# Kernel optimization log

Measured on AMD Instinct MI355X. Metric: run time of the kernel, lower is better.

The kernel has to match this reference:

```python
import jax, jax.numpy as jnp
import numpy as np
import math

NUM_HEADS = 16
CONSTITUENCY_PENALTY = 0.5
CONSTITUENT_BLOCK = 64  # deterministic stand-in for the ChomskyParser constituency spans


def constituency_penalty_mask(seq_len, dtype):
    # Tokens in the same constituent (contiguous block) attend freely;
    # cross-constituent pairs are penalized by CONSTITUENCY_PENALTY.
    blk = jnp.arange(seq_len) // CONSTITUENT_BLOCK
    return jnp.where(blk[:, None] != blk[None, :], CONSTITUENCY_PENALTY, 0.0).astype(dtype)


def setup_inputs() -> dict:
    key = jax.random.key(0)
    ks = jax.random.split(key, 7)
    B, S, H = 8, 1024, 1024
    scale = 1.0 / math.sqrt(H)
    return {
        "hidden_states": jax.random.normal(ks[0], (B, S, H), jnp.float32),
        "Wq": jax.random.normal(ks[1], (H, H), jnp.float32) * scale,
        "bq": jnp.zeros((H,), jnp.float32),
        "Wk": jax.random.normal(ks[2], (H, H), jnp.float32) * scale,
        "bk": jnp.zeros((H,), jnp.float32),
        "Wv": jax.random.normal(ks[3], (H, H), jnp.float32) * scale,
        "bv": jnp.zeros((H,), jnp.float32),
    }


def reference(hidden_states, Wq, bq, Wk, bk, Wv, bv):
    B, S, H = hidden_states.shape
    nh = NUM_HEADS
    hd = H // nh

    def heads(x):  # [B,S,H] -> [B,nh,S,hd]
        return x.reshape(B, S, nh, hd).transpose(0, 2, 1, 3)

    q = heads(hidden_states @ Wq + bq)
    k = heads(hidden_states @ Wk + bk)
    v = heads(hidden_states @ Wv + bv)

    scores = jnp.einsum("bhqd,bhkd->bhqk", q, k) / jnp.sqrt(jnp.asarray(hd, q.dtype))
    # constituency penalty subtracted before softmax (broadcast over batch, heads)
    scores = scores - constituency_penalty_mask(S, scores.dtype)[None, None, :, :]
    probs = jax.nn.softmax(scores, axis=-1)  # dropout is identity in eval

    ctx = jnp.einsum("bhqk,bhkd->bhqd", probs, v)
    ctx = ctx.transpose(0, 2, 1, 3).reshape(B, S, H)
    return ctx
```

## Files before the change

### kernel.cpp

```cpp
#include <hip/hip_runtime.h>
#include <cstdint>

#define BB 8
#define SQ 1024
#define HH 1024
#define NH 16
#define HD 64

typedef __attribute__((ext_vector_type(4))) float f32x4;
typedef __attribute__((ext_vector_type(8))) __bf16 bf16x8;
typedef __attribute__((ext_vector_type(8))) unsigned short u16x8;
typedef __attribute__((ext_vector_type(4))) unsigned short u16x4;

__device__ __forceinline__ unsigned short f2bf(float f){
  uint32_t u = __builtin_bit_cast(uint32_t, f);
  u += 0x7FFFu + ((u >> 16) & 1u);
  return (unsigned short)(u >> 16);
}

__device__ __forceinline__ void gload_lds16(const void* g, void* l){
  __builtin_amdgcn_global_load_lds((__attribute__((address_space(1))) void*)g,
                                   (__attribute__((address_space(3))) void*)l,
                                   16, 0, 0);
}

__global__ __launch_bounds__(256) void k_convert_x(const float* __restrict__ x,
                                                   unsigned short* __restrict__ xb){
  int i = blockIdx.x * 256 + threadIdx.x;
  const f32x4* xv = (const f32x4*)x;
  f32x4 a = xv[2*i], b = xv[2*i+1];
  u16x8 o;
  o[0]=f2bf(a[0]); o[1]=f2bf(a[1]); o[2]=f2bf(a[2]); o[3]=f2bf(a[3]);
  o[4]=f2bf(b[0]); o[5]=f2bf(b[1]); o[6]=f2bf(b[2]); o[7]=f2bf(b[3]);
  ((u16x8*)xb)[i] = o;
}

__global__ __launch_bounds__(256) void k_wt(const float* __restrict__ Wq,
                                            const float* __restrict__ Wk,
                                            const float* __restrict__ Wv,
                                            unsigned short* __restrict__ wt){
  __shared__ float t[32][33];
  int p = blockIdx.z;
  const float* W = (p==0)?Wq:((p==1)?Wk:Wv);
  int n0 = blockIdx.x*32, k0 = blockIdx.y*32;
  int tx = threadIdx.x, ty = threadIdx.y;
  #pragma unroll
  for(int j=0;j<32;j+=8) t[ty+j][tx] = W[(size_t)(k0+ty+j)*HH + n0+tx];
  __syncthreads();
  unsigned short* o = wt + (size_t)p*HH*HH;
  #pragma unroll
  for(int j=0;j<32;j+=8) o[(size_t)(n0+ty+j)*HH + k0+tx] = f2bf(t[tx][ty+j]);
}

#define BM 128
#define BN 128
#define BK 64
__global__ __launch_bounds__(256) void k_qkv(const unsigned short* __restrict__ Xb,
                                             const unsigned short* __restrict__ Wt,
                                             const float* __restrict__ bq,
                                             const float* __restrict__ bk,
                                             const float* __restrict__ bv,
                                             unsigned short* __restrict__ q_ws,
                                             unsigned short* __restrict__ k_ws,
                                             unsigned short* __restrict__ vt_ws){
  __shared__ __align__(16) unsigned short As[BM*BK];
  __shared__ __align__(16) unsigned short Bs[BN*BK];
  int tid = threadIdx.x;
  int lane = tid & 63, wid = tid >> 6;
  int nt = blockIdx.x % 24, mt = blockIdx.x / 24;
  int m0 = mt*BM, n0 = nt*BN;
  int wm = (wid & 1)*64, wn = (wid >> 1)*64;
  int lr = lane & 15, g = lane >> 4;

  const f32x4 zf = {0.f,0.f,0.f,0.f};
  f32x4 acc[4][4];
  #pragma unroll
  for(int a=0;a<4;a++)
    #pragma unroll
    for(int b=0;b<4;b++) acc[a][b] = zf;

  for(int kk=0; kk<1024; kk+=BK){
    __syncthreads();
    #pragma unroll
    for(int it=0; it<4; it++){
      int slot = it*256 + tid;
      int row = slot >> 3, ch = (slot & 7) ^ (row & 7);
      gload_lds16(Xb + (size_t)(m0+row)*1024 + kk + ch*8, &As[slot*8]);
    }
    #pragma unroll
    for(int it=0; it<4; it++){
      int slot = it*256 + tid;
      int row = slot >> 3, ch = (slot & 7) ^ (row & 7);
      gload_lds16(Wt + (size_t)(n0+row)*1024 + kk + ch*8, &Bs[slot*8]);
    }
    __syncthreads();

    #pragma unroll
    for(int ks=0; ks<2; ks++){
      bf16x8 af[4], bfr[4];
      #pragma unroll
      for(int mi=0;mi<4;mi++){
        int r = wm + mi*16 + lr;
        af[mi] = *(const bf16x8*)&As[r*64 + (((ks*4+g) ^ (r&7))<<3)];
      }
      #pragma unroll
      for(int ni=0;ni<4;ni++){
        int r = wn + ni*16 + lr;
        bfr[ni] = *(const bf16x8*)&Bs[r*64 + (((ks*4+g) ^ (r&7))<<3)];
      }
      #pragma unroll
      for(int mi=0;mi<4;mi++)
        #pragma unroll
        for(int ni=0;ni<4;ni++)
          acc[mi][ni] = __builtin_amdgcn_mfma_f32_16x16x32_bf16(af[mi], bfr[ni], acc[mi][ni], 0,0,0);
    }
  }

  int proj = n0 >> 10;
  const float* bias = (proj==0)?bq:((proj==1)?bk:bv);
  const float QSCALE = 0.18033688f;
  #pragma unroll
  for(int mi=0;mi<4;mi++){
    #pragma unroll
    for(int ni=0;ni<4;ni++){
      int ncol = n0 + wn + ni*16 + lr;
      int hcol = ncol & 1023;
      int h = hcol >> 6, d = hcol & 63;
      float bval = bias[hcol];
      if(proj == 0){
        #pragma unroll
        for(int i=0;i<4;i++){
          int m = m0 + wm + mi*16 + g*4 + i;
          int b = m >> 10, s = m & 1023;
          q_ws[((size_t)(b*NH + h)*SQ + s)*HD + d] = f2bf((acc[mi][ni][i] + bval)*QSCALE);
        }
      } else if(proj == 1){
        #pragma unroll
        for(int i=0;i<4;i++){
          int m = m0 + wm + mi*16 + g*4 + i;
          int b = m >> 10, s = m & 1023;
          k_ws[((size_t)(b*NH + h)*SQ + s)*HD + d] = f2bf(acc[mi][ni][i] + bval);
        }
      } else {
        int m = m0 + wm + mi*16 + g*4;
        int b = m >> 10, s = m & 1023;
        u16x4 pk;
        #pragma unroll
        for(int i=0;i<4;i++) pk[i] = f2bf(acc[mi][ni][i] + bval);
        *(u16x4*)&vt_ws[((size_t)(b*NH + h)*HD + d)*SQ + s] = pk;
      }
    }
  }
}

__global__ __launch_bounds__(256) void k_attn(const unsigned short* __restrict__ q_ws,
                                              const unsigned short* __restrict__ k_ws,
                                              const unsigned short* __restrict__ vt_ws,
                                              float* __restrict__ out){
  __shared__ __align__(16) unsigned short Ks[2][64*64];
  __shared__ __align__(16) unsigned short Vs[2][64*64];
  __shared__ __align__(16) unsigned short Ps[4*16*64];
  int tid = threadIdx.x, lane = tid & 63, wid = tid >> 6;
  int lr = lane & 15, g = lane >> 4;
  int qt = blockIdx.x & 15, bh = blockIdx.x >> 4;
  int qbase = qt*64;
  const unsigned short* qp = q_ws + (size_t)bh*SQ*HD;
  const unsigned short* kp = k_ws + (size_t)bh*SQ*HD;
  const unsigned short* vp = vt_ws + (size_t)bh*HD*SQ;

  bf16x8 qf0, qf1;
  {
    size_t qoff = (size_t)(qbase + wid*16 + lr)*HD;
    qf0 = *(const bf16x8*)&qp[qoff + g*8];
    qf1 = *(const bf16x8*)&qp[qoff + 32 + g*8];
  }

  int srow = tid >> 3;
  int sch  = (tid & 7) ^ (srow & 7);

  const f32x4 zf = {0.f,0.f,0.f,0.f};
  float lacc[4];
  f32x4 co[4];
  #pragma unroll
  for(int i=0;i<4;i++) lacc[i] = 0.f;
  #pragma unroll
  for(int dt=0;dt<4;dt++) co[dt] = zf;

  unsigned short* Pw = &Ps[wid*16*64];

  #pragma unroll
  for(int it=0; it<2; it++){
    int row = it*32 + srow, slot = it*256 + tid;
    gload_lds16(kp + (size_t)row*HD + sch*8, &Ks[0][slot*8]);
    gload_lds16(vp + (size_t)row*SQ + sch*8, &Vs[0][slot*8]);
  }
  __syncthreads();

  int cur = 0;
  for(int kt=0; kt<16; kt++){
    if(kt < 15){
      int kb = (kt+1)*64;
      #pragma unroll
      for(int it=0; it<2; it++){
        int row = it*32 + srow, slot = it*256 + tid;
        gload_lds16(kp + (size_t)(kb+row)*HD + sch*8, &Ks[cur^1][slot*8]);
        gload_lds16(vp + (size_t)row*SQ + kb + sch*8, &Vs[cur^1][slot*8]);
      }
    }

    f32x4 sc[4];
    #pragma unroll
    for(int t=0;t<4;t++){
      int r = t*16 + lr;
      bf16x8 kf0 = *(const bf16x8*)&Ks[cur][r*64 + ((g ^ (r&7))<<3)];
      sc[t] = __builtin_amdgcn_mfma_f32_16x16x32_bf16(qf0, kf0, zf, 0,0,0);
      bf16x8 kf1 = *(const bf16x8*)&Ks[cur][r*64 + (((4+g) ^ (r&7))<<3)];
      sc[t] = __builtin_amdgcn_mfma_f32_16x16x32_bf16(qf1, kf1, sc[t], 0,0,0);
    }

    float add = (kt == qt) ? 0.72134752f : 0.0f;
    #pragma unroll
    for(int t=0;t<4;t++){
      int col = t*16 + lr;
      int cc = col >> 3;
      #pragma unroll
      for(int i=0;i<4;i++){
        float pv = __builtin_amdgcn_exp2f(sc[t][i] + add);
        lacc[i] += pv;
        int q = g*4 + i;
        ((__bf16*)Pw)[q*64 + ((cc ^ (q&7))<<3) + (col&7)] = (__bf16)pv;
      }
    }

    #pragma unroll
    for(int dt=0;dt<4;dt++){
      #pragma unroll
      for(int ko=0;ko<2;ko++){
        int cc = ko*4 + g;
        bf16x8 pf = *(const bf16x8*)&Pw[lr*64 + ((cc ^ (lr&7))<<3)];
        int vr = dt*16 + lr;
        bf16x8 vf = *(const bf16x8*)&Vs[cur][vr*64 + ((cc ^ (vr&7))<<3)];
        co[dt] = __builtin_amdgcn_mfma_f32_16x16x32_bf16(pf, vf, co[dt], 0,0,0);
      }
    }

    __syncthreads();
    cur ^= 1;
  }

  float rl[4];
  #pragma unroll
  for(int i=0;i<4;i++){
    float l = lacc[i];
    l += __shfl_xor(l,1); l += __shfl_xor(l,2);
    l += __shfl_xor(l,4); l += __shfl_xor(l,8);
    rl[i] = 1.0f / l;
  }
  int b = bh >> 4, h = bh & 15;
  #pragma unroll
  for(int dt=0;dt<4;dt++){
    #pragma unroll
    for(int i=0;i<4;i++){
      int q = qbase + wid*16 + g*4 + i;
      int d = h*HD + dt*16 + lr;
      out[((size_t)(b*SQ + q))*HH + d] = co[dt][i] * rl[i];
    }
  }
}

extern "C" void kernel_launch(void* const* d_in, const int* in_sizes, int n_in,
                              void* d_out, int out_size, void* d_ws, size_t ws_size,
                              hipStream_t stream){
  const float* hs = (const float*)d_in[0];
  const float* Wq = (const float*)d_in[1];
  const float* bq = (const float*)d_in[2];
  const float* Wk = (const float*)d_in[3];
  const float* bk = (const float*)d_in[4];
  const float* Wv = (const float*)d_in[5];
  const float* bv = (const float*)d_in[6];
  float* out = (float*)d_out;

  unsigned char* ws = (unsigned char*)d_ws;
  const size_t NX = (size_t)8192*1024;
  unsigned short* xb    = (unsigned short*)ws;
  unsigned short* wt    = (unsigned short*)(ws + NX*2);
  unsigned short* q_ws  = (unsigned short*)(ws + NX*2 + (size_t)3*1024*1024*2);
  unsigned short* k_ws  = q_ws + NX;
  unsigned short* vt_ws = k_ws + NX;

  k_convert_x<<<4096, 256, 0, stream>>>(hs, xb);
  k_wt<<<dim3(32,32,3), dim3(32,8), 0, stream>>>(Wq, Wk, Wv, wt);
  k_qkv<<<24*64, 256, 0, stream>>>(xb, wt, bq, bk, bv, q_ws, k_ws, vt_ws);
  k_attn<<<2048, 256, 0, stream>>>(q_ws, k_ws, vt_ws, out);
}
```

Measured before the change: 237.8 us.

## Double-buffer QKV GEMM, swizzle blocks, and widen attention to 32 queries per wave

The QKV projection GEMM now double-buffers its LDS tiles so the next K-slice loads while MFMAs run, and both kernels remap block IDs across XCDs. The attention kernel gives each wave 32 query rows instead of 16, halving the grid so each K/V tile loaded into LDS is reused by more queries. It also computes transposed score tiles (K×Q) so the P stores and output writes are packed vector stores. This doubles LDS and accumulator usage, which may lower occupancy.

```diff
diff --git a/kernel.cpp b/kernel.cpp
--- a/kernel.cpp
+++ b/kernel.cpp
@@ -63,15 +63,20 @@
                                              unsigned short* __restrict__ q_ws,
                                              unsigned short* __restrict__ k_ws,
                                              unsigned short* __restrict__ vt_ws){
-  __shared__ __align__(16) unsigned short As[BM*BK];
-  __shared__ __align__(16) unsigned short Bs[BN*BK];
+  __shared__ __align__(16) unsigned short As[2][BM*BK];
+  __shared__ __align__(16) unsigned short Bs[2][BN*BK];
   int tid = threadIdx.x;
   int lane = tid & 63, wid = tid >> 6;
-  int nt = blockIdx.x % 24, mt = blockIdx.x / 24;
+  int bid = blockIdx.x;
+  int sw = (bid & 7)*192 + (bid >> 3);
+  int nt = sw % 24, mt = sw / 24;
   int m0 = mt*BM, n0 = nt*BN;
   int wm = (wid & 1)*64, wn = (wid >> 1)*64;
   int lr = lane & 15, g = lane >> 4;
 
+  int srow = tid >> 3;
+  int sch  = (tid & 7) ^ (srow & 7);
+
   const f32x4 zf = {0.f,0.f,0.f,0.f};
   f32x4 acc[4][4];
   #pragma unroll
@@ -79,34 +84,37 @@
     #pragma unroll
     for(int b=0;b<4;b++) acc[a][b] = zf;
 
-  for(int kk=0; kk<1024; kk+=BK){
-    __syncthreads();
-    #pragma unroll
-    for(int it=0; it<4; it++){
-      int slot = it*256 + tid;
-      int row = slot >> 3, ch = (slot & 7) ^ (row & 7);
-      gload_lds16(Xb + (size_t)(m0+row)*1024 + kk + ch*8, &As[slot*8]);
-    }
-    #pragma unroll
-    for(int it=0; it<4; it++){
-      int slot = it*256 + tid;
-      int row = slot >> 3, ch = (slot & 7) ^ (row & 7);
-      gload_lds16(Wt + (size_t)(n0+row)*1024 + kk + ch*8, &Bs[slot*8]);
-    }
-    __syncthreads();
-
+  #pragma unroll
+  for(int it=0; it<4; it++){
+    int row = it*32 + srow, slot = it*256 + tid;
+    gload_lds16(Xb + (size_t)(m0+row)*1024 + sch*8, &As[0][slot*8]);
+    gload_lds16(Wt + (size_t)(n0+row)*1024 + sch*8, &Bs[0][slot*8]);
+  }
+  __syncthreads();
+
+  int cur = 0;
+  for(int kk=0; kk<16; kk++){
+    if(kk < 15){
+      int kb = (kk+1)*BK;
+      #pragma unroll
+      for(int it=0; it<4; it++){
+        int row = it*32 + srow, slot = it*256 + tid;
+        gload_lds16(Xb + (size_t)(m0+row)*1024 + kb + sch*8, &As[cur^1][slot*8]);
+        gload_lds16(Wt + (size_t)(n0+row)*1024 + kb + sch*8, &Bs[cur^1][slot*8]);
+      }
+    }
     #pragma unroll
     for(int ks=0; ks<2; ks++){
       bf16x8 af[4], bfr[4];
       #pragma unroll
       for(int mi=0;mi<4;mi++){
         int r = wm + mi*16 + lr;
-        af[mi] = *(const bf16x8*)&As[r*64 + (((ks*4+g) ^ (r&7))<<3)];
+        af[mi] = *(const bf16x8*)&As[cur][r*64 + (((ks*4+g) ^ (r&7))<<3)];
       }
       #pragma unroll
       for(int ni=0;ni<4;ni++){
         int r = wn + ni*16 + lr;
-        bfr[ni] = *(const bf16x8*)&Bs[r*64 + (((ks*4+g) ^ (r&7))<<3)];
+        bfr[ni] = *(const bf16x8*)&Bs[cur][r*64 + (((ks*4+g) ^ (r&7))<<3)];
       }
       #pragma unroll
       for(int mi=0;mi<4;mi++)
@@ -114,6 +122,8 @@
         for(int ni=0;ni<4;ni++)
           acc[mi][ni] = __builtin_amdgcn_mfma_f32_16x16x32_bf16(af[mi], bfr[ni], acc[mi][ni], 0,0,0);
     }
+    __syncthreads();
+    cur ^= 1;
   }
 
   int proj = n0 >> 10;
@@ -159,34 +169,38 @@
                                               float* __restrict__ out){
   __shared__ __align__(16) unsigned short Ks[2][64*64];
   __shared__ __align__(16) unsigned short Vs[2][64*64];
-  __shared__ __align__(16) unsigned short Ps[4*16*64];
+  __shared__ __align__(16) unsigned short Ps[4][32*64];
   int tid = threadIdx.x, lane = tid & 63, wid = tid >> 6;
   int lr = lane & 15, g = lane >> 4;
-  int qt = blockIdx.x & 15, bh = blockIdx.x >> 4;
-  int qbase = qt*64;
+  int bid = blockIdx.x;
+  int swz = (bid & 7)*128 + (bid >> 3);
+  int qb = swz & 7, bh = swz >> 3;
+  int qw = qb*128 + wid*32;
   const unsigned short* qp = q_ws + (size_t)bh*SQ*HD;
   const unsigned short* kp = k_ws + (size_t)bh*SQ*HD;
   const unsigned short* vp = vt_ws + (size_t)bh*HD*SQ;
 
-  bf16x8 qf0, qf1;
-  {
-    size_t qoff = (size_t)(qbase + wid*16 + lr)*HD;
-    qf0 = *(const bf16x8*)&qp[qoff + g*8];
-    qf1 = *(const bf16x8*)&qp[qoff + 32 + g*8];
-  }
+  bf16x8 qf[2][2];
+  #pragma unroll
+  for(int ns=0;ns<2;ns++)
+    #pragma unroll
+    for(int ks=0;ks<2;ks++)
+      qf[ns][ks] = *(const bf16x8*)&qp[(size_t)(qw + ns*16 + lr)*HD + ks*32 + g*8];
+
+  int diag = qw >> 6;
 
   int srow = tid >> 3;
   int sch  = (tid & 7) ^ (srow & 7);
 
   const f32x4 zf = {0.f,0.f,0.f,0.f};
-  float lacc[4];
-  f32x4 co[4];
-  #pragma unroll
-  for(int i=0;i<4;i++) lacc[i] = 0.f;
-  #pragma unroll
-  for(int dt=0;dt<4;dt++) co[dt] = zf;
-
-  unsigned short* Pw = &Ps[wid*16*64];
+  float lacc[2] = {0.f, 0.f};
+  f32x4 co[4][2];
+  #pragma unroll
+  for(int ms=0;ms<4;ms++)
+    #pragma unroll
+    for(int ns=0;ns<2;ns++) co[ms][ns] = zf;
+
+  unsigned short* Pw = &Ps[wid][0];
 
   #pragma unroll
   for(int it=0; it<2; it++){
@@ -208,39 +222,50 @@
       }
     }
 
-    f32x4 sc[4];
-    #pragma unroll
-    for(int t=0;t<4;t++){
-      int r = t*16 + lr;
+    f32x4 sc[4][2];
+    #pragma unroll
+    for(int ms=0;ms<4;ms++){
+      int r = ms*16 + lr;
       bf16x8 kf0 = *(const bf16x8*)&Ks[cur][r*64 + ((g ^ (r&7))<<3)];
-      sc[t] = __builtin_amdgcn_mfma_f32_16x16x32_bf16(qf0, kf0, zf, 0,0,0);
       bf16x8 kf1 = *(const bf16x8*)&Ks[cur][r*64 + (((4+g) ^ (r&7))<<3)];
-      sc[t] = __builtin_amdgcn_mfma_f32_16x16x32_bf16(qf1, kf1, sc[t], 0,0,0);
-    }
-
-    float add = (kt == qt) ? 0.72134752f : 0.0f;
-    #pragma unroll
-    for(int t=0;t<4;t++){
-      int col = t*16 + lr;
-      int cc = col >> 3;
-      #pragma unroll
-      for(int i=0;i<4;i++){
-        float pv = __builtin_amdgcn_exp2f(sc[t][i] + add);
-        lacc[i] += pv;
-        int q = g*4 + i;
-        ((__bf16*)Pw)[q*64 + ((cc ^ (q&7))<<3) + (col&7)] = (__bf16)pv;
-      }
-    }
-
-    #pragma unroll
-    for(int dt=0;dt<4;dt++){
-      #pragma unroll
-      for(int ko=0;ko<2;ko++){
-        int cc = ko*4 + g;
-        bf16x8 pf = *(const bf16x8*)&Pw[lr*64 + ((cc ^ (lr&7))<<3)];
-        int vr = dt*16 + lr;
-        bf16x8 vf = *(const bf16x8*)&Vs[cur][vr*64 + ((cc ^ (vr&7))<<3)];
-        co[dt] = __builtin_amdgcn_mfma_f32_16x16x32_bf16(pf, vf, co[dt], 0,0,0);
+      #pragma unroll
+      for(int ns=0;ns<2;ns++){
+        sc[ms][ns] = __builtin_amdgcn_mfma_f32_16x16x32_bf16(kf0, qf[ns][0], zf, 0,0,0);
+        sc[ms][ns] = __builtin_amdgcn_mfma_f32_16x16x32_bf16(kf1, qf[ns][1], sc[ms][ns], 0,0,0);
+      }
+    }
+
+    float add = (kt == diag) ? 0.72134752f : 0.0f;
+
+    #pragma unroll
+    for(int ms=0;ms<4;ms++){
+      #pragma unroll
+      for(int ns=0;ns<2;ns++){
+        u16x4 pk;
+        #pragma unroll
+        for(int i=0;i<4;i++){
+          float pv = __builtin_amdgcn_exp2f(sc[ms][ns][i] + add);
+          lacc[ns] += pv;
+          pk[i] = f2bf(pv);
+        }
+        int q = ns*16 + lr;
+        int c = ms*2 + (g>>1);
+        *(u16x4*)&Pw[q*64 + ((c ^ (q&7))<<3) + (g&1)*4] = pk;
+      }
+    }
+
+    #pragma unroll
+    for(int ms=0;ms<4;ms++){
+      int vr = ms*16 + lr;
+      bf16x8 vf0 = *(const bf16x8*)&Vs[cur][vr*64 + ((g ^ (vr&7))<<3)];
+      bf16x8 vf1 = *(const bf16x8*)&Vs[cur][vr*64 + (((4+g) ^ (vr&7))<<3)];
+      #pragma unroll
+      for(int ns=0;ns<2;ns++){
+        int q = ns*16 + lr;
+        bf16x8 pf0 = *(const bf16x8*)&Pw[q*64 + ((g ^ (q&7))<<3)];
+        bf16x8 pf1 = *(const bf16x8*)&Pw[q*64 + (((4+g) ^ (q&7))<<3)];
+        co[ms][ns] = __builtin_amdgcn_mfma_f32_16x16x32_bf16(vf0, pf0, co[ms][ns], 0,0,0);
+        co[ms][ns] = __builtin_amdgcn_mfma_f32_16x16x32_bf16(vf1, pf1, co[ms][ns], 0,0,0);
       }
     }
 
@@ -248,22 +273,24 @@
     cur ^= 1;
   }
 
-  float rl[4];
-  #pragma unroll
-  for(int i=0;i<4;i++){
-    float l = lacc[i];
-    l += __shfl_xor(l,1); l += __shfl_xor(l,2);
-    l += __shfl_xor(l,4); l += __shfl_xor(l,8);
-    rl[i] = 1.0f / l;
+  float rl[2];
+  #pragma unroll
+  for(int ns=0;ns<2;ns++){
+    float l = lacc[ns];
+    l += __shfl_xor(l, 16);
+    l += __shfl_xor(l, 32);
+    rl[ns] = 1.0f / l;
   }
   int b = bh >> 4, h = bh & 15;
   #pragma unroll
-  for(int dt=0;dt<4;dt++){
-    #pragma unroll
-    for(int i=0;i<4;i++){
-      int q = qbase + wid*16 + g*4 + i;
-      int d = h*HD + dt*16 + lr;
-      out[((size_t)(b*SQ + q))*HH + d] = co[dt][i] * rl[i];
+  for(int ms=0;ms<4;ms++){
+    #pragma unroll
+    for(int ns=0;ns<2;ns++){
+      int q = qw + ns*16 + lr;
+      int d = h*HD + ms*16 + g*4;
+      f32x4 r = co[ms][ns];
+      r[0]*=rl[ns]; r[1]*=rl[ns]; r[2]*=rl[ns]; r[3]*=rl[ns];
+      *(f32x4*)&out[((size_t)(b*SQ + q))*HH + d] = r;
     }
   }
 }
@@ -291,5 +318,5 @@
   k_convert_x<<<4096, 256, 0, stream>>>(hs, xb);
   k_wt<<<dim3(32,32,3), dim3(32,8), 0, stream>>>(Wq, Wk, Wv, wt);
   k_qkv<<<24*64, 256, 0, stream>>>(xb, wt, bq, bk, bv, q_ws, k_ws, vt_ws);
-  k_attn<<<2048, 256, 0, stream>>>(q_ws, k_ws, vt_ws, out);
-}
+  k_attn<<<1024, 256, 0, stream>>>(q_ws, k_ws, vt_ws, out);
+}
```

Result: faster. 226.4 us (-4.8%).
